# Kernel tuning notes

Hardware: AMD Instinct MI355X
Metric: run time of the kernel (lower is better)

Reference implementation:

```python
import jax, jax.numpy as jnp
import numpy as np

B, N, M = 4, 1024, 3072          # batch, latent (query) len, prefix context len
D, H, DH, L, F = 512, 8, 64, 6, 2048  # dim, heads, dim_head, depth, ff hidden
SCALE = DH ** -0.5


def _ln(x, g, b):
    m = jnp.mean(x, axis=-1, keepdims=True)
    v = jnp.mean(jnp.square(x - m), axis=-1, keepdims=True)
    return (x - m) * jax.lax.rsqrt(v + 1e-5) * g + b


def _heads(t):  # [b, n, h*d] -> [b, h, n, d]
    b, n, _ = t.shape
    return t.reshape(b, n, H, DH).transpose(0, 2, 1, 3)


def _attend(q, k, v):
    # q:[b,h,i,d], k/v:[b,h,j,d]; causal mask triu(j-i+1) as in source
    i, j = q.shape[2], k.shape[2]
    sim = jnp.einsum('bhid,bhjd->bhij', q * SCALE, k)
    mask = jnp.triu(jnp.ones((i, j), dtype=bool), j - i + 1)
    sim = jnp.where(mask, -jnp.finfo(sim.dtype).max, sim)
    attn = jax.nn.softmax(sim, axis=-1)
    out = jnp.einsum('bhij,bhjd->bhid', attn, v)
    return out.transpose(0, 2, 1, 3).reshape(q.shape[0], i, H * DH)


def _ff(x, g, b, w1, w2):
    return jax.nn.gelu(_ln(x, g, b) @ w1, approximate=False) @ w2


def setup_inputs() -> dict:
    key = jax.random.key(0)
    ks = jax.random.split(key, 12)
    rn = lambda k, shape: jax.random.normal(k, shape, dtype=jnp.float32) * 0.02
    return {
        'x': jax.random.normal(ks[0], (B, N, D), jnp.float32),
        'context': jax.random.normal(ks[1], (B, M, D), jnp.float32),
        'pa_norm_g': jnp.ones((D,), jnp.float32), 'pa_norm_b': jnp.zeros((D,), jnp.float32),
        'pa_cnorm_g': jnp.ones((D,), jnp.float32), 'pa_cnorm_b': jnp.zeros((D,), jnp.float32),
        'pa_wq': rn(ks[2], (D, H * DH)), 'pa_wkv': rn(ks[3], (D, 2 * H * DH)),
        'pa_wo': rn(ks[4], (H * DH, D)), 'pa_wo_b': jnp.zeros((D,), jnp.float32),
        'pf_ln_g': jnp.ones((D,), jnp.float32), 'pf_ln_b': jnp.zeros((D,), jnp.float32),
        'pf_w1': rn(ks[5], (D, F)), 'pf_w2': rn(ks[6], (F, D)),
        'sa_ln_g': jnp.ones((L, D), jnp.float32), 'sa_ln_b': jnp.zeros((L, D), jnp.float32),
        'sa_wqkv': rn(ks[7], (L, D, 3 * H * DH)), 'sa_wo': rn(ks[8], (L, H * DH, D)),
        'sf_ln_g': jnp.ones((L, D), jnp.float32), 'sf_ln_b': jnp.zeros((L, D), jnp.float32),
        'sf_w1': rn(ks[9], (L, D, F)), 'sf_w2': rn(ks[10], (L, F, D)),
    }


def reference(x, context, pa_norm_g, pa_norm_b, pa_cnorm_g, pa_cnorm_b,
              pa_wq, pa_wkv, pa_wo, pa_wo_b, pf_ln_g, pf_ln_b, pf_w1, pf_w2,
              sa_ln_g, sa_ln_b, sa_wqkv, sa_wo, sf_ln_g, sf_ln_b, sf_w1, sf_w2):
    # --- CausalPrefixAttention (eval mode: no dropout, context_mask=None) ---
    xn = _ln(x, pa_norm_g, pa_norm_b)
    cn = _ln(context, pa_cnorm_g, pa_cnorm_b)
    q = _heads(xn @ pa_wq)
    k_in, v_in = jnp.split(xn @ pa_wkv, 2, axis=-1)
    k_c, v_c = jnp.split(cn @ pa_wkv, 2, axis=-1)
    k = _heads(jnp.concatenate([k_c, k_in], axis=1))  # [b,h,M+N,d]
    v = _heads(jnp.concatenate([v_c, v_in], axis=1))
    x = _attend(q, k, v) @ pa_wo + pa_wo_b + x
    x = _ff(x, pf_ln_g, pf_ln_b, pf_w1, pf_w2) + x
    # --- depth x (CausalAttention + FeedForward) ---
    for l in range(L):
        xn = _ln(x, sa_ln_g[l], sa_ln_b[l])
        qq, kk, vv = jnp.split(xn @ sa_wqkv[l], 3, axis=-1)
        x = _attend(_heads(qq), _heads(kk), _heads(vv)) @ sa_wo[l] + x
        x = _ff(x, sf_ln_g[l], sf_ln_b[l], sf_w1[l], sf_w2[l]) + x
    return x
```

## Files before the change

kernel.cpp:

```cpp
#include <hip/hip_runtime.h>
#include <hip/hip_bf16.h>
#include <cstdint>
#include <cstddef>

typedef __bf16 bf16;
typedef __attribute__((ext_vector_type(8))) __bf16 bf16x8;
typedef __attribute__((ext_vector_type(4))) __bf16 bf16x4;
typedef __attribute__((ext_vector_type(4))) float f32x4;

constexpr int B_ = 4, QN = 1024, MCTX = 3072, D_ = 512, H_ = 8, DHE = 64, L_ = 6, FF_ = 2048;
constexpr float SCL2_ = 0.18033688011f;

__device__ __forceinline__ f32x4 mfma16(bf16x8 a, bf16x8 b, f32x4 c) {
  return __builtin_amdgcn_mfma_f32_16x16x32_bf16(a, b, c, 0, 0, 0);
}

__device__ __forceinline__ void gl_lds16(const bf16* g, bf16* l) {
  __builtin_amdgcn_global_load_lds((const __attribute__((address_space(1))) void*)g,
                                   (__attribute__((address_space(3))) void*)l, 16, 0, 0);
}

__device__ __forceinline__ float fexp2(float x) {
  float r;
  asm("v_exp_f32 %0, %1" : "=v"(r) : "v"(x));
  return r;
}

__global__ __launch_bounds__(256) void ln_kernel(const float* __restrict__ x,
                                                 const float* __restrict__ g,
                                                 const float* __restrict__ b,
                                                 bf16* __restrict__ out, int rows) {
  int wid = threadIdx.x >> 6, lane = threadIdx.x & 63;
  int row = blockIdx.x * 4 + wid;
  if (row >= rows) return;
  const float* xr = x + (size_t)row * D_;
  f32x4 a0 = *(const f32x4*)(xr + lane * 8);
  f32x4 a1 = *(const f32x4*)(xr + lane * 8 + 4);
  float s = 0.f;
#pragma unroll
  for (int i = 0; i < 4; i++) { s += a0[i]; s += a1[i]; }
#pragma unroll
  for (int d = 1; d < 64; d <<= 1) s += __shfl_xor(s, d);
  float mean = s * (1.0f / 512.0f);
  float q = 0.f;
#pragma unroll
  for (int i = 0; i < 4; i++) {
    float t0 = a0[i] - mean, t1 = a1[i] - mean;
    q += t0 * t0 + t1 * t1;
  }
#pragma unroll
  for (int d = 1; d < 64; d <<= 1) q += __shfl_xor(q, d);
  float rstd = rsqrtf(q * (1.0f / 512.0f) + 1e-5f);
  f32x4 g0 = *(const f32x4*)(g + lane * 8);
  f32x4 g1 = *(const f32x4*)(g + lane * 8 + 4);
  f32x4 b0 = *(const f32x4*)(b + lane * 8);
  f32x4 b1 = *(const f32x4*)(b + lane * 8 + 4);
  bf16x8 o;
#pragma unroll
  for (int i = 0; i < 4; i++) {
    o[i] = (bf16)((a0[i] - mean) * rstd * g0[i] + b0[i]);
    o[i + 4] = (bf16)((a1[i] - mean) * rstd * g1[i] + b1[i]);
  }
  *(bf16x8*)(out + (size_t)row * D_ + lane * 8) = o;
}

struct WDesc { const float* src; bf16* dst; int K; int N; int tstart; };
struct WPack { WDesc d[30]; int n; };

__global__ __launch_bounds__(256) void wtrans_all(WPack p) {
  __shared__ float tile[64][65];
  const int bid = blockIdx.x;
  int mi = 0;
  for (int i = 1; i < p.n; i++)
    if (p.d[i].tstart <= bid) mi = i;
  const float* src = p.d[mi].src;
  bf16* dst = p.d[mi].dst;
  const int K = p.d[mi].K, N = p.d[mi].N;
  const int lt = bid - p.d[mi].tstart;
  const int ntx = N >> 6;
  const int n0 = (lt % ntx) * 64, k0 = (lt / ntx) * 64;
  const int tx = threadIdx.x, ty = threadIdx.y;
#pragma unroll
  for (int pp = 0; pp < 16; pp++)
    tile[pp * 4 + ty][tx] = src[(size_t)(k0 + pp * 4 + ty) * N + n0 + tx];
  __syncthreads();
#pragma unroll
  for (int pp = 0; pp < 16; pp++)
    dst[(size_t)(n0 + pp * 4 + ty) * K + k0 + tx] = (bf16)tile[tx][pp * 4 + ty];
}

template <int EPI>
__global__ __launch_bounds__(256) void gemm128(const bf16* __restrict__ A,
                                               const bf16* __restrict__ BT,
                                               void* __restrict__ C0,
                                               void* __restrict__ C1,
                                               void* __restrict__ C2,
                                               const float* __restrict__ resid,
                                               const float* __restrict__ bias,
                                               int M, int N, int K, int vstr) {
  __shared__ bf16 sm[6 * 4096];
  bf16* sA = sm;
  bf16* sB = sm + 3 * 4096;
  const int tid = threadIdx.x, wid = tid >> 6, lane = tid & 63;
  const int lr = lane & 15, lg = lane >> 4;
  const int tm = blockIdx.y * 128, tn = blockIdx.x * 128;
  const int wr = (wid >> 1) * 64, wc = (wid & 1) * 64;

  const int r0 = tid >> 2, ls0 = tid & 3;
  const int gs0 = ls0 ^ (r0 & 3);
  const bf16* gA0 = A + (size_t)(tm + r0) * K + gs0 * 8;
  const bf16* gB0 = BT + (size_t)(tn + r0) * K + gs0 * 8;
  const bf16* gA1 = gA0 + (size_t)64 * K;
  const bf16* gB1 = gB0 + (size_t)64 * K;

  f32x4 acc[4][4] = {};
  const int nt = K >> 5;

  auto stage = [&](int bi, int kt) {
    gl_lds16(gA0 + kt, sA + bi * 4096 + tid * 8);
    gl_lds16(gA1 + kt, sA + bi * 4096 + (tid + 256) * 8);
    gl_lds16(gB0 + kt, sB + bi * 4096 + tid * 8);
    gl_lds16(gB1 + kt, sB + bi * 4096 + (tid + 256) * 8);
  };

  stage(0, 0);
  stage(1, 32);

  for (int t = 0; t < nt; ++t) {
    const int bi = t % 3;
    if (t + 1 < nt) {
      asm volatile("s_waitcnt vmcnt(4)" ::: "memory");
    } else {
      asm volatile("s_waitcnt vmcnt(0)" ::: "memory");
    }
    __builtin_amdgcn_s_barrier();
    __builtin_amdgcn_sched_barrier(0);
    if (t + 2 < nt) stage((t + 2) % 3, (t + 2) * 32);

    bf16x8 af[4], bfr[4];
#pragma unroll
    for (int i = 0; i < 4; i++) {
      const int row = wr + i * 16 + lr;
      af[i] = *(const bf16x8*)&sA[bi * 4096 + row * 32 + ((lg ^ (row & 3)) * 8)];
    }
#pragma unroll
    for (int j = 0; j < 4; j++) {
      const int row = wc + j * 16 + lr;
      bfr[j] = *(const bf16x8*)&sB[bi * 4096 + row * 32 + ((lg ^ (row & 3)) * 8)];
    }
#pragma unroll
    for (int i = 0; i < 4; i++)
#pragma unroll
      for (int j = 0; j < 4; j++)
        acc[i][j] = mfma16(af[i], bfr[j], acc[i][j]);
  }

  const bool row_major_dst =
      (EPI == 1) || (EPI == 3 && tn < 1024) || (EPI == 4 && tn < 1024) || (EPI == 5 && tn < 512);
  if (row_major_dst) {
    bf16* dst;
    int dstr, rbase, coff;
    if (EPI == 1) { dst = (bf16*)C0; dstr = N; rbase = tm; coff = tn; }
    else if (EPI == 3) {
      if (tn < 512) { dst = (bf16*)C0; dstr = 512; rbase = tm; coff = tn; }
      else { dst = (bf16*)C1; dstr = 1024; rbase = (tm >> 10) * 4096 + (tm & 1023) + 3072; coff = tn - 512; }
    } else if (EPI == 4) { dst = (bf16*)C0; dstr = 1536; rbase = tm; coff = tn; }
    else { dst = (bf16*)C1; dstr = 1024; rbase = (tm / 3072) * 4096 + (tm % 3072); coff = tn; }

    __syncthreads();
    bf16* lb = sm;
#pragma unroll
    for (int i = 0; i < 4; i++) {
#pragma unroll
      for (int r = 0; r < 4; r++) {
        const int row = wr + i * 16 + lg * 4 + r;
#pragma unroll
        for (int j = 0; j < 4; j++) {
          const int col = wc + j * 16 + lr;
          float v = acc[i][j][r];
          if (EPI == 1) {
            float u = v * (0.7978845608f + 0.0356774081f * v * v);
            float e = fexp2(fminf(2.885390082f * u, 80.0f));
            v = v * e / (1.0f + e);
          }
          lb[row * 128 + (col ^ ((row & 7) << 3))] = (bf16)v;
        }
      }
    }
    __syncthreads();
#pragma unroll
    for (int p = 0; p < 8; p++) {
      const int row = p * 16 + (tid >> 4);
      const int cb = (tid & 15) * 8;
      bf16x8 v = *(const bf16x8*)&lb[row * 128 + (cb ^ ((row & 7) << 3))];
      *(bf16x8*)&dst[(size_t)(rbase + row) * dstr + coff + cb] = v;
    }
  } else {
#pragma unroll
    for (int i = 0; i < 4; i++) {
      const int row = tm + wr + i * 16 + lg * 4;
#pragma unroll
      for (int j = 0; j < 4; j++) {
        const int col = tn + wc + j * 16 + lr;
        bf16x4 pk = {(bf16)acc[i][j][0], (bf16)acc[i][j][1],
                     (bf16)acc[i][j][2], (bf16)acc[i][j][3]};
        if (EPI == 3) {
          const int cc = col - 1024, hh = cc >> 6, dh = cc & 63;
          const int bb = row >> 10, s = (row & 1023) + 3072;
          *(bf16x4*)&((bf16*)C2)[((size_t)(bb * 8 + hh) * 64 + dh) * vstr + s] = pk;
        } else if (EPI == 4) {
          const int cc = col - 1024, hh = cc >> 6, dh = cc & 63;
          const int bb = row >> 10, s = row & 1023;
          *(bf16x4*)&((bf16*)C2)[((size_t)(bb * 8 + hh) * 64 + dh) * vstr + s] = pk;
        } else {
          const int bq = row / 3072, s = row - bq * 3072;
          const int cc = col - 512, hh = cc >> 6, dh = cc & 63;
          *(bf16x4*)&((bf16*)C2)[((size_t)(bq * 8 + hh) * 64 + dh) * vstr + s] = pk;
        }
      }
    }
  }
}

__global__ __launch_bounds__(512) void gemm64k2(const bf16* __restrict__ A,
                                                const bf16* __restrict__ BT,
                                                float* __restrict__ Cout,
                                                const float* __restrict__ resid,
                                                const float* __restrict__ bias,
                                                int M, int N, int K) {
  __shared__ bf16 sm[2][2][64 * 128];
  const int tid = threadIdx.x, wid = tid >> 6, lane = tid & 63;
  const int lr = lane & 15, lg = lane >> 4;
  const int tm = blockIdx.y * 64, tn = blockIdx.x * 64;
  const int ws = wid >> 2;
  const int wq = wid & 3;
  const int wr = (wq >> 1) * 32, wc = (wq & 1) * 32;

  const int r0 = tid >> 4, u0 = tid & 7, h0 = (tid >> 3) & 1;
  const int g0 = h0 * 8 + (u0 ^ (r0 & 7));
  const bf16* gA0 = A + (size_t)(tm + r0) * K + g0 * 8;
  const bf16* gB0 = BT + (size_t)(tn + r0) * K + g0 * 8;
  const bf16* gA1 = gA0 + (size_t)32 * K;
  const bf16* gB1 = gB0 + (size_t)32 * K;

  auto stage = [&](int bi, int kt) {
    gl_lds16(gA0 + kt, &sm[bi][0][tid * 8]);
    gl_lds16(gA1 + kt, &sm[bi][0][(tid + 512) * 8]);
    gl_lds16(gB0 + kt, &sm[bi][1][tid * 8]);
    gl_lds16(gB1 + kt, &sm[bi][1][(tid + 512) * 8]);
  };

  f32x4 acc[2][2] = {};
  const int nt = K >> 7;
  stage(0, 0);
  int buf = 0;
  for (int t = 0; t < nt; ++t) {
    asm volatile("s_waitcnt vmcnt(0)" ::: "memory");
    __builtin_amdgcn_s_barrier();
    __builtin_amdgcn_sched_barrier(0);
    if (t + 1 < nt) stage(buf ^ 1, (t + 1) * 128);

    bf16x8 af[2][2], bfr[2][2];
#pragma unroll
    for (int i = 0; i < 2; i++) {
      const int row = wr + i * 16 + lr;
#pragma unroll
      for (int kk = 0; kk < 2; kk++) {
        const int slot = ws * 8 + ((kk * 4 + lg) ^ (row & 7));
        af[i][kk] = *(const bf16x8*)&sm[buf][0][row * 128 + slot * 8];
      }
    }
#pragma unroll
    for (int j = 0; j < 2; j++) {
      const int row = wc + j * 16 + lr;
#pragma unroll
      for (int kk = 0; kk < 2; kk++) {
        const int slot = ws * 8 + ((kk * 4 + lg) ^ (row & 7));
        bfr[j][kk] = *(const bf16x8*)&sm[buf][1][row * 128 + slot * 8];
      }
    }
#pragma unroll
    for (int kk = 0; kk < 2; kk++)
#pragma unroll
      for (int i = 0; i < 2; i++)
#pragma unroll
        for (int j = 0; j < 2; j++)
          acc[i][j] = mfma16(af[i][kk], bfr[j][kk], acc[i][j]);
    buf ^= 1;
  }

  __syncthreads();
  float* lbuf = (float*)&sm[0][0][0];
  if (ws == 0) {
#pragma unroll
    for (int i = 0; i < 2; i++)
#pragma unroll
      for (int r = 0; r < 4; r++) {
        const int row = wr + i * 16 + lg * 4 + r;
#pragma unroll
        for (int j = 0; j < 2; j++)
          lbuf[row * 68 + wc + j * 16 + lr] = acc[i][j][r];
      }
  }
  __syncthreads();
  if (ws == 1) {
#pragma unroll
    for (int i = 0; i < 2; i++)
#pragma unroll
      for (int r = 0; r < 4; r++) {
        const int row = wr + i * 16 + lg * 4 + r;
#pragma unroll
        for (int j = 0; j < 2; j++)
          lbuf[row * 68 + wc + j * 16 + lr] += acc[i][j][r];
      }
  }
  __syncthreads();
#pragma unroll
  for (int p = 0; p < 2; p++) {
    const int row = p * 32 + (tid >> 4);
    const int col = (tid & 15) * 4;
    f32x4 v = *(const f32x4*)&lbuf[row * 68 + col];
    const size_t gidx = (size_t)(tm + row) * N + tn + col;
    f32x4 rs = *(const f32x4*)&resid[gidx];
    if (bias) {
      f32x4 bs = *(const f32x4*)&bias[tn + col];
#pragma unroll
      for (int e = 0; e < 4; e++) v[e] += bs[e];
    }
#pragma unroll
    for (int e = 0; e < 4; e++) v[e] += rs[e];
    *(f32x4*)&Cout[gidx] = v;
  }
}

template <int NSPLIT>
__global__ __launch_bounds__(512) void attn_kernel(const bf16* __restrict__ q, int qstride,
                                                   const bf16* __restrict__ k, int kstride,
                                                   const bf16* __restrict__ vt,
                                                   bf16* __restrict__ out,
                                                   bf16* __restrict__ po,
                                                   float* __restrict__ pm,
                                                   float* __restrict__ pl,
                                                   int Skv, int Moff, int spllen) {
  __shared__ bf16 kls[2][4096];
  __shared__ bf16 vls[2][4096];
  __shared__ bf16 pls[8][1024];

  const int tid = threadIdx.x, wid = tid >> 6, lane = tid & 63;
  const int lr = lane & 15, lg = lane >> 4, lg4 = lg * 4;
  const int b = blockIdx.z, h = blockIdx.y;
  const int qblk = blockIdx.x / NSPLIT;
  const int split = blockIdx.x % NSPLIT;
  const int q0b = qblk * 128;
  const int q0w = q0b + wid * 16;
  const int kv_lo = split * spllen;

  int jhi_blk = Moff + q0b + 127;
  if (jhi_blk > Skv - 1) jhi_blk = Skv - 1;
  int hi = kv_lo + spllen;
  if (hi > jhi_blk + 1) hi = jhi_blk + 1;
  const int ntl = (hi > kv_lo) ? ((hi - kv_lo + 63) >> 6) : 0;

  if (NSPLIT > 1 && ntl == 0) {
    size_t rb = ((size_t)split * B_ * H_ + (size_t)b * H_ + h) * QN + q0w;
    const int row = lane >> 2;
    bf16x8 z = {};
#pragma unroll
    for (int half = 0; half < 2; half++)
      *(bf16x8*)&po[(rb + row) * 64 + (lane & 3) * 16 + half * 8] = z;
    if (lg == 0) { pm[rb + lr] = -3e38f; pl[rb + lr] = 0.f; }
    return;
  }

  const int sel = ((tid >> 6) & 1) * 32 + ((tid >> 4) & 3) * 8;
  const int srow0 = (tid >> 7) * 16 + (tid & 15);
  const bf16* kbase = k + (size_t)b * Skv * kstride + h * DHE + sel;
  const bf16* vbase = vt + (size_t)((b * H_ + h) * DHE) * Skv + sel;

  const bf16* qp = q + (size_t)(b * QN + q0w + lr) * qstride + h * DHE;
  bf16x8 qa0 = *(const bf16x8*)(qp + lg * 8);
  bf16x8 qa1 = *(const bf16x8*)(qp + 32 + lg * 8);
#pragma unroll
  for (int i = 0; i < 8; i++) {
    qa0[i] = (bf16)((float)qa0[i] * SCL2_);
    qa1[i] = (bf16)((float)qa1[i] * SCL2_);
  }
  bf16x8 vones;
#pragma unroll
  for (int i = 0; i < 8; i++) vones[i] = (bf16)1.0f;

  f32x4 o[4] = {};
  f32x4 o4 = {};

  auto stage = [&](int bi, int j0) {
    gl_lds16(kbase + (size_t)(j0 + srow0) * kstride, &kls[bi][tid * 8]);
    gl_lds16(vbase + (size_t)srow0 * Skv + j0, &vls[bi][tid * 8]);
  };

  stage(0, kv_lo);
  __syncthreads();
  int buf = 0;
  bf16* pw = &pls[wid][0];

  for (int t = 0; t < ntl; ++t) {
    const int j0 = kv_lo + t * 64;
    if (t + 1 < ntl) stage(buf ^ 1, j0 + 64);
    const bf16* kbp = &kls[buf][0];
    const bf16* vbp = &vls[buf][0];

    f32x4 sv[4];
    __builtin_amdgcn_s_setprio(1);
#pragma unroll
    for (int kg = 0; kg < 4; kg++) {
      bf16x8 k0 = *(const bf16x8*)(kbp + (kg * 128 + lane) * 8);
      bf16x8 k1 = *(const bf16x8*)(kbp + (kg * 128 + 64 + lane) * 8);
      f32x4 z = {0.f, 0.f, 0.f, 0.f};
      z = mfma16(k0, qa0, z);
      z = mfma16(k1, qa1, z);
      sv[kg] = z;
    }
    __builtin_amdgcn_s_setprio(0);
    const bool full = (j0 + 63 <= Moff + q0w);
    if (!full) {
      const int limq = Moff + q0w + lr;
#pragma unroll
      for (int kg = 0; kg < 4; kg++)
#pragma unroll
        for (int r = 0; r < 4; r++)
          if (j0 + kg * 16 + lg4 + r > limq) sv[kg][r] = -3e38f;
    }
#pragma unroll
    for (int kg = 0; kg < 4; kg++) {
      float p0 = fexp2(sv[kg][0]);
      float p1 = fexp2(sv[kg][1]);
      float p2 = fexp2(sv[kg][2]);
      float p3 = fexp2(sv[kg][3]);
      bf16x4 pk = {(bf16)p0, (bf16)p1, (bf16)p2, (bf16)p3};
      const int k8 = kg * 2 + (lg >> 1);
      *(bf16x4*)(pw + ((k8 >> 2) * 64 + (k8 & 3) * 16 + lr) * 8 + (lg & 1) * 4) = pk;
    }
    bf16x8 pa0 = *(const bf16x8*)(pw + lane * 8);
    bf16x8 pa1 = *(const bf16x8*)(pw + (64 + lane) * 8);
    __builtin_amdgcn_s_setprio(1);
#pragma unroll
    for (int f = 0; f < 4; f++) {
      bf16x8 v0 = *(const bf16x8*)(vbp + (f * 128 + lane) * 8);
      bf16x8 v1 = *(const bf16x8*)(vbp + (f * 128 + 64 + lane) * 8);
      o[f] = mfma16(pa0, v0, o[f]);
      o[f] = mfma16(pa1, v1, o[f]);
    }
    o4 = mfma16(pa0, vones, o4);
    o4 = mfma16(pa1, vones, o4);
    __builtin_amdgcn_s_setprio(0);
    __syncthreads();
    buf ^= 1;
  }

  if (NSPLIT == 1) {
    float li[4];
#pragma unroll
    for (int r = 0; r < 4; r++) li[r] = 1.0f / o4[r];
#pragma unroll
    for (int f = 0; f < 4; f++)
#pragma unroll
      for (int r = 0; r < 4; r++) {
        const int row = lg4 + r, col = f * 16 + lr;
        pw[row * 64 + (col ^ ((row & 7) << 3))] = (bf16)(o[f][r] * li[r]);
      }
    const int row = lane >> 2;
#pragma unroll
    for (int half = 0; half < 2; half++) {
      const int cb = (lane & 3) * 16 + half * 8;
      bf16x8 v = *(const bf16x8*)&pw[row * 64 + (cb ^ ((row & 7) << 3))];
      *(bf16x8*)&out[(size_t)(b * QN + q0w + row) * D_ + h * DHE + cb] = v;
    }
  } else {
    size_t rb = ((size_t)split * B_ * H_ + (size_t)b * H_ + h) * QN + q0w;
#pragma unroll
    for (int f = 0; f < 4; f++)
#pragma unroll
      for (int r = 0; r < 4; r++) {
        const int row = lg4 + r, col = f * 16 + lr;
        pw[row * 64 + (col ^ ((row & 7) << 3))] = (bf16)o[f][r];
      }
    const int row = lane >> 2;
#pragma unroll
    for (int half = 0; half < 2; half++) {
      const int cb = (lane & 3) * 16 + half * 8;
      bf16x8 v = *(const bf16x8*)&pw[row * 64 + (cb ^ ((row & 7) << 3))];
      *(bf16x8*)&po[(rb + row) * 64 + cb] = v;
    }
    if (lr == 0) {
#pragma unroll
      for (int r = 0; r < 4; r++) {
        pm[rb + lg4 + r] = 0.f;
        pl[rb + lg4 + r] = o4[r];
      }
    }
  }
}

template <int NSPLIT>
__global__ __launch_bounds__(256) void attn_combine(const bf16* __restrict__ po,
                                                    const float* __restrict__ pm,
                                                    const float* __restrict__ pl,
                                                    bf16* __restrict__ out) {
  constexpr int TOT = B_ * H_ * QN;
  const int wid = threadIdx.x >> 6, lane = threadIdx.x & 63;
  const int row = blockIdx.x * 4 + wid;
  float mv[NSPLIT], lv[NSPLIT];
  float mstar = -3e38f;
#pragma unroll
  for (int s = 0; s < NSPLIT; s++) {
    mv[s] = pm[s * TOT + row];
    lv[s] = pl[s * TOT + row];
    mstar = fmaxf(mstar, mv[s]);
  }
  float lstar = 0.f, acc = 0.f;
#pragma unroll
  for (int s = 0; s < NSPLIT; s++) {
    float w = fexp2(mv[s] - mstar);
    lstar += lv[s] * w;
    acc += (float)po[((size_t)s * TOT + row) * 64 + lane] * w;
  }
  const int b = row >> 13, hq = row & 8191, h = hq >> 10, qq = hq & 1023;
  out[((size_t)b * QN + qq) * D_ + h * DHE + lane] = (bf16)(acc / lstar);
}

extern "C" void kernel_launch(void* const* d_in, const int* in_sizes, int n_in,
                              void* d_out, int out_size, void* d_ws, size_t ws_size,
                              hipStream_t stream) {
  const float* x       = (const float*)d_in[0];
  const float* ctx     = (const float*)d_in[1];
  const float* pa_ng   = (const float*)d_in[2];
  const float* pa_nb   = (const float*)d_in[3];
  const float* pa_cg   = (const float*)d_in[4];
  const float* pa_cb   = (const float*)d_in[5];
  const float* pa_wq   = (const float*)d_in[6];
  const float* pa_wkv  = (const float*)d_in[7];
  const float* pa_wo   = (const float*)d_in[8];
  const float* pa_wob  = (const float*)d_in[9];
  const float* pf_g    = (const float*)d_in[10];
  const float* pf_b    = (const float*)d_in[11];
  const float* pf_w1   = (const float*)d_in[12];
  const float* pf_w2   = (const float*)d_in[13];
  const float* sa_g    = (const float*)d_in[14];
  const float* sa_b    = (const float*)d_in[15];
  const float* sa_wqkv = (const float*)d_in[16];
  const float* sa_wo   = (const float*)d_in[17];
  const float* sf_g    = (const float*)d_in[18];
  const float* sf_b    = (const float*)d_in[19];
  const float* sf_w1   = (const float*)d_in[20];
  const float* sf_w2   = (const float*)d_in[21];
  float* xo = (float*)d_out;

  char* ws = (char*)d_ws;
  size_t off = 0;
  auto alloc = [&](size_t bytes) -> char* {
    char* p = ws + off;
    off += (bytes + 255) & ~(size_t)255;
    return p;
  };

  bf16* wqT    = (bf16*)alloc((size_t)512 * 512 * 2);
  bf16* wkvT   = (bf16*)alloc((size_t)1024 * 512 * 2);
  bf16* woT    = (bf16*)alloc((size_t)512 * 512 * 2);
  bf16* w1T    = (bf16*)alloc((size_t)2048 * 512 * 2);
  bf16* w2T    = (bf16*)alloc((size_t)512 * 2048 * 2);
  bf16* saqkvT = (bf16*)alloc((size_t)L_ * 1536 * 512 * 2);
  bf16* sawoT  = (bf16*)alloc((size_t)L_ * 512 * 512 * 2);
  bf16* sfw1T  = (bf16*)alloc((size_t)L_ * 2048 * 512 * 2);
  bf16* sfw2T  = (bf16*)alloc((size_t)L_ * 512 * 2048 * 2);
  bf16* xn    = (bf16*)alloc((size_t)4096 * 512 * 2);
  bf16* reg1  = (bf16*)alloc((size_t)12288 * 512 * 2);
  bf16* qb    = (bf16*)alloc((size_t)4096 * 512 * 2);
  bf16* reg2  = (bf16*)alloc((size_t)B_ * 4096 * 1024 * 2);
  bf16* vtb   = (bf16*)alloc((size_t)B_ * H_ * 64 * 4096 * 2);
  bf16* attnb = (bf16*)alloc((size_t)4096 * 512 * 2);
  constexpr int NSPL = 4;
  constexpr int TOTR = B_ * H_ * QN;
  bf16* po = (bf16*)alloc((size_t)NSPL * TOTR * 64 * 2);
  float* pmb = (float*)alloc((size_t)NSPL * TOTR * 4);
  float* plb = (float*)alloc((size_t)NSPL * TOTR * 4);
  const bool use_split = (off <= ws_size);
  bf16* cn = reg1;
  bf16* qkvb = reg1;
  bf16* kvb = reg2;
  bf16* ffh = reg2;
  (void)in_sizes; (void)n_in; (void)out_size;

  WPack wp;
  int nt_acc = 0, wi = 0;
  auto addw = [&](const float* s, bf16* d, int K, int N) {
    wp.d[wi].src = s; wp.d[wi].dst = d; wp.d[wi].K = K; wp.d[wi].N = N;
    wp.d[wi].tstart = nt_acc;
    nt_acc += (N / 64) * (K / 64);
    wi++;
  };
  addw(pa_wq, wqT, 512, 512);
  addw(pa_wkv, wkvT, 512, 1024);
  addw(pa_wo, woT, 512, 512);
  addw(pf_w1, w1T, 512, 2048);
  addw(pf_w2, w2T, 2048, 512);
  for (int l = 0; l < L_; l++) {
    addw(sa_wqkv + (size_t)l * 512 * 1536, saqkvT + (size_t)l * 1536 * 512, 512, 1536);
    addw(sa_wo + (size_t)l * 512 * 512, sawoT + (size_t)l * 512 * 512, 512, 512);
    addw(sf_w1 + (size_t)l * 512 * 2048, sfw1T + (size_t)l * 2048 * 512, 512, 2048);
    addw(sf_w2 + (size_t)l * 2048 * 512, sfw2T + (size_t)l * 512 * 2048, 2048, 512);
  }
  wp.n = wi;
  wtrans_all<<<nt_acc, dim3(64, 4, 1), 0, stream>>>(wp);

  ln_kernel<<<1024, 256, 0, stream>>>(x, pa_ng, pa_nb, xn, 4096);
  ln_kernel<<<3072, 256, 0, stream>>>(ctx, pa_cg, pa_cb, cn, 12288);
  hipLaunchKernelGGL(HIP_KERNEL_NAME(gemm128<5>), dim3(1024 / 128, 12288 / 128), dim3(256), 0,
                     stream, cn, wkvT, nullptr, kvb, vtb, nullptr, nullptr, 12288, 1024, 512, 4096);
  hipLaunchKernelGGL(HIP_KERNEL_NAME(gemm128<3>), dim3(1536 / 128, 4096 / 128), dim3(256), 0,
                     stream, xn, wqT, qb, kvb, vtb, nullptr, nullptr, 4096, 1536, 512, 4096);
  if (use_split) {
    hipLaunchKernelGGL(HIP_KERNEL_NAME(attn_kernel<NSPL>), dim3((QN / 128) * NSPL, H_, B_), dim3(512), 0,
                       stream, qb, 512, kvb, 1024, vtb, attnb, po, pmb, plb, 4096, MCTX, 1024);
    hipLaunchKernelGGL(HIP_KERNEL_NAME(attn_combine<NSPL>), dim3(TOTR / 4), dim3(256), 0,
                       stream, po, pmb, plb, attnb);
  } else {
    hipLaunchKernelGGL(HIP_KERNEL_NAME(attn_kernel<1>), dim3(QN / 128, H_, B_), dim3(512), 0,
                       stream, qb, 512, kvb, 1024, vtb, attnb, po, pmb, plb, 4096, MCTX, 4096);
  }
  gemm64k2<<<dim3(512 / 64, 4096 / 64), 512, 0, stream>>>(attnb, woT, xo, x, pa_wob, 4096, 512, 512);
  ln_kernel<<<1024, 256, 0, stream>>>(xo, pf_g, pf_b, xn, 4096);
  hipLaunchKernelGGL(HIP_KERNEL_NAME(gemm128<1>), dim3(2048 / 128, 4096 / 128), dim3(256), 0,
                     stream, xn, w1T, ffh, nullptr, nullptr, nullptr, nullptr, 4096, 2048, 512, 0);
  gemm64k2<<<dim3(512 / 64, 4096 / 64), 512, 0, stream>>>(ffh, w2T, xo, xo, nullptr, 4096, 512, 2048);

  for (int l = 0; l < L_; l++) {
    ln_kernel<<<1024, 256, 0, stream>>>(xo, sa_g + l * 512, sa_b + l * 512, xn, 4096);
    hipLaunchKernelGGL(HIP_KERNEL_NAME(gemm128<4>), dim3(1536 / 128, 4096 / 128), dim3(256), 0,
                       stream, xn, saqkvT + (size_t)l * 1536 * 512, qkvb, nullptr, vtb,
                       nullptr, nullptr, 4096, 1536, 512, 1024);
    if (use_split) {
      hipLaunchKernelGGL(HIP_KERNEL_NAME(attn_kernel<2>), dim3((QN / 128) * 2, H_, B_), dim3(512), 0,
                         stream, qkvb, 1536, qkvb + 512, 1536, vtb, attnb, po, pmb, plb, 1024, 0, 512);
      hipLaunchKernelGGL(HIP_KERNEL_NAME(attn_combine<2>), dim3(TOTR / 4), dim3(256), 0,
                         stream, po, pmb, plb, attnb);
    } else {
      hipLaunchKernelGGL(HIP_KERNEL_NAME(attn_kernel<1>), dim3(QN / 128, H_, B_), dim3(512), 0,
                         stream, qkvb, 1536, qkvb + 512, 1536, vtb, attnb, po, pmb, plb, 1024, 0, 1024);
    }
    gemm64k2<<<dim3(512 / 64, 4096 / 64), 512, 0, stream>>>(attnb, sawoT + (size_t)l * 512 * 512,
                                                            xo, xo, nullptr, 4096, 512, 512);
    ln_kernel<<<1024, 256, 0, stream>>>(xo, sf_g + l * 512, sf_b + l * 512, xn, 4096);
    hipLaunchKernelGGL(HIP_KERNEL_NAME(gemm128<1>), dim3(2048 / 128, 4096 / 128), dim3(256), 0,
                       stream, xn, sfw1T + (size_t)l * 2048 * 512, ffh, nullptr, nullptr,
                       nullptr, nullptr, 4096, 2048, 512, 0);
    gemm64k2<<<dim3(512 / 64, 4096 / 64), 512, 0, stream>>>(ffh, sfw2T + (size_t)l * 512 * 2048,
                                                            xo, xo, nullptr, 4096, 512, 2048);
  }
}
```

Measured before the change: 752.7 us.

## Fuse split-KV attention combine into attention kernel; triple-buffer gemm64k2 K loop

The separate attn_combine launch is removed. Each split block now publishes its partial output and row sum, then bumps a per-group atomic counter, and the last block to arrive reduces the splits and writes the final output. The unused running-max buffer is dropped and counters are zeroed once with a memset. Separately, gemm64k2 moves from a double-buffered 128-wide K tile to a triple-buffered 64-wide K tile with vmcnt(2) waits, so loads stay in flight across iterations. This trades the extra kernel launches and combine passes for atomics and threadfences, and adds more barrier iterations in the GEMM.

```diff
diff --git a/kernel.cpp b/kernel.cpp
--- a/kernel.cpp
+++ b/kernel.cpp
@@ -228,7 +228,7 @@
                                                 const float* __restrict__ resid,
                                                 const float* __restrict__ bias,
                                                 int M, int N, int K) {
-  __shared__ bf16 sm[2][2][64 * 128];
+  __shared__ bf16 sm[3][2][64 * 64];
   const int tid = threadIdx.x, wid = tid >> 6, lane = tid & 63;
   const int lr = lane & 15, lg = lane >> 4;
   const int tm = blockIdx.y * 64, tn = blockIdx.x * 64;
@@ -236,57 +236,48 @@
   const int wq = wid & 3;
   const int wr = (wq >> 1) * 32, wc = (wq & 1) * 32;
 
-  const int r0 = tid >> 4, u0 = tid & 7, h0 = (tid >> 3) & 1;
-  const int g0 = h0 * 8 + (u0 ^ (r0 & 7));
+  const int r0 = tid >> 3, u0 = tid & 7;
+  const int g0 = u0 ^ (r0 & 7);
   const bf16* gA0 = A + (size_t)(tm + r0) * K + g0 * 8;
   const bf16* gB0 = BT + (size_t)(tn + r0) * K + g0 * 8;
-  const bf16* gA1 = gA0 + (size_t)32 * K;
-  const bf16* gB1 = gB0 + (size_t)32 * K;
 
   auto stage = [&](int bi, int kt) {
     gl_lds16(gA0 + kt, &sm[bi][0][tid * 8]);
-    gl_lds16(gA1 + kt, &sm[bi][0][(tid + 512) * 8]);
     gl_lds16(gB0 + kt, &sm[bi][1][tid * 8]);
-    gl_lds16(gB1 + kt, &sm[bi][1][(tid + 512) * 8]);
   };
 
   f32x4 acc[2][2] = {};
-  const int nt = K >> 7;
+  const int nt = K >> 6;
   stage(0, 0);
-  int buf = 0;
+  if (nt > 1) stage(1, 64);
+
   for (int t = 0; t < nt; ++t) {
-    asm volatile("s_waitcnt vmcnt(0)" ::: "memory");
+    const int bi = t % 3;
+    if (t + 1 < nt) {
+      asm volatile("s_waitcnt vmcnt(2)" ::: "memory");
+    } else {
+      asm volatile("s_waitcnt vmcnt(0)" ::: "memory");
+    }
     __builtin_amdgcn_s_barrier();
     __builtin_amdgcn_sched_barrier(0);
-    if (t + 1 < nt) stage(buf ^ 1, (t + 1) * 128);
-
-    bf16x8 af[2][2], bfr[2][2];
+    if (t + 2 < nt) stage((t + 2) % 3, (t + 2) * 64);
+
+    bf16x8 af[2], bfr[2];
 #pragma unroll
     for (int i = 0; i < 2; i++) {
       const int row = wr + i * 16 + lr;
-#pragma unroll
-      for (int kk = 0; kk < 2; kk++) {
-        const int slot = ws * 8 + ((kk * 4 + lg) ^ (row & 7));
-        af[i][kk] = *(const bf16x8*)&sm[buf][0][row * 128 + slot * 8];
-      }
+      af[i] = *(const bf16x8*)&sm[bi][0][row * 64 + (((ws * 4 + lg) ^ (row & 7)) * 8)];
     }
 #pragma unroll
     for (int j = 0; j < 2; j++) {
       const int row = wc + j * 16 + lr;
-#pragma unroll
-      for (int kk = 0; kk < 2; kk++) {
-        const int slot = ws * 8 + ((kk * 4 + lg) ^ (row & 7));
-        bfr[j][kk] = *(const bf16x8*)&sm[buf][1][row * 128 + slot * 8];
-      }
-    }
-#pragma unroll
-    for (int kk = 0; kk < 2; kk++)
-#pragma unroll
-      for (int i = 0; i < 2; i++)
-#pragma unroll
-        for (int j = 0; j < 2; j++)
-          acc[i][j] = mfma16(af[i][kk], bfr[j][kk], acc[i][j]);
-    buf ^= 1;
+      bfr[j] = *(const bf16x8*)&sm[bi][1][row * 64 + (((ws * 4 + lg) ^ (row & 7)) * 8)];
+    }
+#pragma unroll
+    for (int i = 0; i < 2; i++)
+#pragma unroll
+      for (int j = 0; j < 2; j++)
+        acc[i][j] = mfma16(af[i], bfr[j], acc[i][j]);
   }
 
   __syncthreads();
@@ -339,12 +330,13 @@
                                                    const bf16* __restrict__ vt,
                                                    bf16* __restrict__ out,
                                                    bf16* __restrict__ po,
-                                                   float* __restrict__ pm,
                                                    float* __restrict__ pl,
+                                                   unsigned* __restrict__ cnt,
                                                    int Skv, int Moff, int spllen) {
   __shared__ bf16 kls[2][4096];
   __shared__ bf16 vls[2][4096];
   __shared__ bf16 pls[8][1024];
+  __shared__ unsigned scnt_sh;
 
   const int tid = threadIdx.x, wid = tid >> 6, lane = tid & 63;
   const int lr = lane & 15, lg = lane >> 4, lg4 = lg * 4;
@@ -354,6 +346,7 @@
   const int q0b = qblk * 128;
   const int q0w = q0b + wid * 16;
   const int kv_lo = split * spllen;
+  constexpr int TOT = B_ * H_ * QN;
 
   int jhi_blk = Moff + q0b + 127;
   if (jhi_blk > Skv - 1) jhi_blk = Skv - 1;
@@ -362,169 +355,176 @@
   const int ntl = (hi > kv_lo) ? ((hi - kv_lo + 63) >> 6) : 0;
 
   if (NSPLIT > 1 && ntl == 0) {
-    size_t rb = ((size_t)split * B_ * H_ + (size_t)b * H_ + h) * QN + q0w;
+    size_t rb = ((size_t)split * TOT + (size_t)(b * H_ + h) * QN + q0w);
     const int row = lane >> 2;
     bf16x8 z = {};
 #pragma unroll
     for (int half = 0; half < 2; half++)
       *(bf16x8*)&po[(rb + row) * 64 + (lane & 3) * 16 + half * 8] = z;
-    if (lg == 0) { pm[rb + lr] = -3e38f; pl[rb + lr] = 0.f; }
-    return;
-  }
-
-  const int sel = ((tid >> 6) & 1) * 32 + ((tid >> 4) & 3) * 8;
-  const int srow0 = (tid >> 7) * 16 + (tid & 15);
-  const bf16* kbase = k + (size_t)b * Skv * kstride + h * DHE + sel;
-  const bf16* vbase = vt + (size_t)((b * H_ + h) * DHE) * Skv + sel;
-
-  const bf16* qp = q + (size_t)(b * QN + q0w + lr) * qstride + h * DHE;
-  bf16x8 qa0 = *(const bf16x8*)(qp + lg * 8);
-  bf16x8 qa1 = *(const bf16x8*)(qp + 32 + lg * 8);
-#pragma unroll
-  for (int i = 0; i < 8; i++) {
-    qa0[i] = (bf16)((float)qa0[i] * SCL2_);
-    qa1[i] = (bf16)((float)qa1[i] * SCL2_);
-  }
-  bf16x8 vones;
-#pragma unroll
-  for (int i = 0; i < 8; i++) vones[i] = (bf16)1.0f;
-
-  f32x4 o[4] = {};
-  f32x4 o4 = {};
-
-  auto stage = [&](int bi, int j0) {
-    gl_lds16(kbase + (size_t)(j0 + srow0) * kstride, &kls[bi][tid * 8]);
-    gl_lds16(vbase + (size_t)srow0 * Skv + j0, &vls[bi][tid * 8]);
-  };
-
-  stage(0, kv_lo);
-  __syncthreads();
-  int buf = 0;
-  bf16* pw = &pls[wid][0];
-
-  for (int t = 0; t < ntl; ++t) {
-    const int j0 = kv_lo + t * 64;
-    if (t + 1 < ntl) stage(buf ^ 1, j0 + 64);
-    const bf16* kbp = &kls[buf][0];
-    const bf16* vbp = &vls[buf][0];
-
-    f32x4 sv[4];
-    __builtin_amdgcn_s_setprio(1);
-#pragma unroll
-    for (int kg = 0; kg < 4; kg++) {
-      bf16x8 k0 = *(const bf16x8*)(kbp + (kg * 128 + lane) * 8);
-      bf16x8 k1 = *(const bf16x8*)(kbp + (kg * 128 + 64 + lane) * 8);
-      f32x4 z = {0.f, 0.f, 0.f, 0.f};
-      z = mfma16(k0, qa0, z);
-      z = mfma16(k1, qa1, z);
-      sv[kg] = z;
-    }
-    __builtin_amdgcn_s_setprio(0);
-    const bool full = (j0 + 63 <= Moff + q0w);
-    if (!full) {
-      const int limq = Moff + q0w + lr;
-#pragma unroll
-      for (int kg = 0; kg < 4; kg++)
-#pragma unroll
-        for (int r = 0; r < 4; r++)
-          if (j0 + kg * 16 + lg4 + r > limq) sv[kg][r] = -3e38f;
-    }
-#pragma unroll
-    for (int kg = 0; kg < 4; kg++) {
-      float p0 = fexp2(sv[kg][0]);
-      float p1 = fexp2(sv[kg][1]);
-      float p2 = fexp2(sv[kg][2]);
-      float p3 = fexp2(sv[kg][3]);
-      bf16x4 pk = {(bf16)p0, (bf16)p1, (bf16)p2, (bf16)p3};
-      const int k8 = kg * 2 + (lg >> 1);
-      *(bf16x4*)(pw + ((k8 >> 2) * 64 + (k8 & 3) * 16 + lr) * 8 + (lg & 1) * 4) = pk;
-    }
-    bf16x8 pa0 = *(const bf16x8*)(pw + lane * 8);
-    bf16x8 pa1 = *(const bf16x8*)(pw + (64 + lane) * 8);
-    __builtin_amdgcn_s_setprio(1);
-#pragma unroll
-    for (int f = 0; f < 4; f++) {
-      bf16x8 v0 = *(const bf16x8*)(vbp + (f * 128 + lane) * 8);
-      bf16x8 v1 = *(const bf16x8*)(vbp + (f * 128 + 64 + lane) * 8);
-      o[f] = mfma16(pa0, v0, o[f]);
-      o[f] = mfma16(pa1, v1, o[f]);
-    }
-    o4 = mfma16(pa0, vones, o4);
-    o4 = mfma16(pa1, vones, o4);
-    __builtin_amdgcn_s_setprio(0);
+    if (lr == 0) {
+#pragma unroll
+      for (int r = 0; r < 4; r++) pl[rb + lg4 + r] = 0.f;
+    }
+  } else {
+    const int sel = ((tid >> 6) & 1) * 32 + ((tid >> 4) & 3) * 8;
+    const int srow0 = (tid >> 7) * 16 + (tid & 15);
+    const bf16* kbase = k + (size_t)b * Skv * kstride + h * DHE + sel;
+    const bf16* vbase = vt + (size_t)((b * H_ + h) * DHE) * Skv + sel;
+
+    const bf16* qp = q + (size_t)(b * QN + q0w + lr) * qstride + h * DHE;
+    bf16x8 qa0 = *(const bf16x8*)(qp + lg * 8);
+    bf16x8 qa1 = *(const bf16x8*)(qp + 32 + lg * 8);
+#pragma unroll
+    for (int i = 0; i < 8; i++) {
+      qa0[i] = (bf16)((float)qa0[i] * SCL2_);
+      qa1[i] = (bf16)((float)qa1[i] * SCL2_);
+    }
+    bf16x8 vones;
+#pragma unroll
+    for (int i = 0; i < 8; i++) vones[i] = (bf16)1.0f;
+
+    f32x4 o[4] = {};
+    f32x4 o4 = {};
+
+    auto stage = [&](int bi, int j0) {
+      gl_lds16(kbase + (size_t)(j0 + srow0) * kstride, &kls[bi][tid * 8]);
+      gl_lds16(vbase + (size_t)srow0 * Skv + j0, &vls[bi][tid * 8]);
+    };
+
+    stage(0, kv_lo);
     __syncthreads();
-    buf ^= 1;
-  }
-
-  if (NSPLIT == 1) {
-    float li[4];
-#pragma unroll
-    for (int r = 0; r < 4; r++) li[r] = 1.0f / o4[r];
-#pragma unroll
-    for (int f = 0; f < 4; f++)
-#pragma unroll
-      for (int r = 0; r < 4; r++) {
-        const int row = lg4 + r, col = f * 16 + lr;
-        pw[row * 64 + (col ^ ((row & 7) << 3))] = (bf16)(o[f][r] * li[r]);
-      }
-    const int row = lane >> 2;
-#pragma unroll
-    for (int half = 0; half < 2; half++) {
-      const int cb = (lane & 3) * 16 + half * 8;
-      bf16x8 v = *(const bf16x8*)&pw[row * 64 + (cb ^ ((row & 7) << 3))];
-      *(bf16x8*)&out[(size_t)(b * QN + q0w + row) * D_ + h * DHE + cb] = v;
-    }
-  } else {
-    size_t rb = ((size_t)split * B_ * H_ + (size_t)b * H_ + h) * QN + q0w;
-#pragma unroll
-    for (int f = 0; f < 4; f++)
-#pragma unroll
-      for (int r = 0; r < 4; r++) {
-        const int row = lg4 + r, col = f * 16 + lr;
-        pw[row * 64 + (col ^ ((row & 7) << 3))] = (bf16)o[f][r];
-      }
-    const int row = lane >> 2;
-#pragma unroll
-    for (int half = 0; half < 2; half++) {
-      const int cb = (lane & 3) * 16 + half * 8;
-      bf16x8 v = *(const bf16x8*)&pw[row * 64 + (cb ^ ((row & 7) << 3))];
-      *(bf16x8*)&po[(rb + row) * 64 + cb] = v;
-    }
-    if (lr == 0) {
-#pragma unroll
-      for (int r = 0; r < 4; r++) {
-        pm[rb + lg4 + r] = 0.f;
-        pl[rb + lg4 + r] = o4[r];
-      }
-    }
-  }
-}
-
-template <int NSPLIT>
-__global__ __launch_bounds__(256) void attn_combine(const bf16* __restrict__ po,
-                                                    const float* __restrict__ pm,
-                                                    const float* __restrict__ pl,
-                                                    bf16* __restrict__ out) {
-  constexpr int TOT = B_ * H_ * QN;
-  const int wid = threadIdx.x >> 6, lane = threadIdx.x & 63;
-  const int row = blockIdx.x * 4 + wid;
-  float mv[NSPLIT], lv[NSPLIT];
-  float mstar = -3e38f;
-#pragma unroll
-  for (int s = 0; s < NSPLIT; s++) {
-    mv[s] = pm[s * TOT + row];
-    lv[s] = pl[s * TOT + row];
-    mstar = fmaxf(mstar, mv[s]);
-  }
-  float lstar = 0.f, acc = 0.f;
-#pragma unroll
-  for (int s = 0; s < NSPLIT; s++) {
-    float w = fexp2(mv[s] - mstar);
-    lstar += lv[s] * w;
-    acc += (float)po[((size_t)s * TOT + row) * 64 + lane] * w;
-  }
-  const int b = row >> 13, hq = row & 8191, h = hq >> 10, qq = hq & 1023;
-  out[((size_t)b * QN + qq) * D_ + h * DHE + lane] = (bf16)(acc / lstar);
+    int buf = 0;
+    bf16* pw = &pls[wid][0];
+
+    for (int t = 0; t < ntl; ++t) {
+      const int j0 = kv_lo + t * 64;
+      if (t + 1 < ntl) stage(buf ^ 1, j0 + 64);
+      const bf16* kbp = &kls[buf][0];
+      const bf16* vbp = &vls[buf][0];
+
+      f32x4 sv[4];
+      __builtin_amdgcn_s_setprio(1);
+#pragma unroll
+      for (int kg = 0; kg < 4; kg++) {
+        bf16x8 k0 = *(const bf16x8*)(kbp + (kg * 128 + lane) * 8);
+        bf16x8 k1 = *(const bf16x8*)(kbp + (kg * 128 + 64 + lane) * 8);
+        f32x4 z = {0.f, 0.f, 0.f, 0.f};
+        z = mfma16(k0, qa0, z);
+        z = mfma16(k1, qa1, z);
+        sv[kg] = z;
+      }
+      __builtin_amdgcn_s_setprio(0);
+      const bool full = (j0 + 63 <= Moff + q0w);
+      if (!full) {
+        const int limq = Moff + q0w + lr;
+#pragma unroll
+        for (int kg = 0; kg < 4; kg++)
+#pragma unroll
+          for (int r = 0; r < 4; r++)
+            if (j0 + kg * 16 + lg4 + r > limq) sv[kg][r] = -3e38f;
+      }
+#pragma unroll
+      for (int kg = 0; kg < 4; kg++) {
+        float p0 = fexp2(sv[kg][0]);
+        float p1 = fexp2(sv[kg][1]);
+        float p2 = fexp2(sv[kg][2]);
+        float p3 = fexp2(sv[kg][3]);
+        bf16x4 pk = {(bf16)p0, (bf16)p1, (bf16)p2, (bf16)p3};
+        const int k8 = kg * 2 + (lg >> 1);
+        *(bf16x4*)(pw + ((k8 >> 2) * 64 + (k8 & 3) * 16 + lr) * 8 + (lg & 1) * 4) = pk;
+      }
+      bf16x8 pa0 = *(const bf16x8*)(pw + lane * 8);
+      bf16x8 pa1 = *(const bf16x8*)(pw + (64 + lane) * 8);
+      __builtin_amdgcn_s_setprio(1);
+#pragma unroll
+      for (int f = 0; f < 4; f++) {
+        bf16x8 v0 = *(const bf16x8*)(vbp + (f * 128 + lane) * 8);
+        bf16x8 v1 = *(const bf16x8*)(vbp + (f * 128 + 64 + lane) * 8);
+        o[f] = mfma16(pa0, v0, o[f]);
+        o[f] = mfma16(pa1, v1, o[f]);
+      }
+      o4 = mfma16(pa0, vones, o4);
+      o4 = mfma16(pa1, vones, o4);
+      __builtin_amdgcn_s_setprio(0);
+      __syncthreads();
+      buf ^= 1;
+    }
+
+    if (NSPLIT == 1) {
+      float li[4];
+#pragma unroll
+      for (int r = 0; r < 4; r++) li[r] = 1.0f / o4[r];
+#pragma unroll
+      for (int f = 0; f < 4; f++)
+#pragma unroll
+        for (int r = 0; r < 4; r++) {
+          const int row = lg4 + r, col = f * 16 + lr;
+          pw[row * 64 + (col ^ ((row & 7) << 3))] = (bf16)(o[f][r] * li[r]);
+        }
+      const int row = lane >> 2;
+#pragma unroll
+      for (int half = 0; half < 2; half++) {
+        const int cb = (lane & 3) * 16 + half * 8;
+        bf16x8 v = *(const bf16x8*)&pw[row * 64 + (cb ^ ((row & 7) << 3))];
+        *(bf16x8*)&out[(size_t)(b * QN + q0w + row) * D_ + h * DHE + cb] = v;
+      }
+    } else {
+      size_t rb = ((size_t)split * TOT + (size_t)(b * H_ + h) * QN + q0w);
+#pragma unroll
+      for (int f = 0; f < 4; f++)
+#pragma unroll
+        for (int r = 0; r < 4; r++) {
+          const int row = lg4 + r, col = f * 16 + lr;
+          pw[row * 64 + (col ^ ((row & 7) << 3))] = (bf16)o[f][r];
+        }
+      const int row = lane >> 2;
+#pragma unroll
+      for (int half = 0; half < 2; half++) {
+        const int cb = (lane & 3) * 16 + half * 8;
+        bf16x8 v = *(const bf16x8*)&pw[row * 64 + (cb ^ ((row & 7) << 3))];
+        *(bf16x8*)&po[(rb + row) * 64 + cb] = v;
+      }
+      if (lr == 0) {
+#pragma unroll
+        for (int r = 0; r < 4; r++) pl[rb + lg4 + r] = o4[r];
+      }
+    }
+  }
+
+  if (NSPLIT > 1) {
+    __threadfence();
+    __syncthreads();
+    if (tid == 0)
+      scnt_sh = atomicAdd(&cnt[(unsigned)((b * H_ + h) * (QN / 128) + qblk)], 1u);
+    __syncthreads();
+    if (scnt_sh == NSPLIT - 1) {
+      __threadfence();
+      const int row = tid >> 2;
+      const int cb = (tid & 3) * 16;
+      const size_t base = (size_t)(b * H_ + h) * QN + q0b + row;
+      float l = 0.f;
+      float a0[8] = {}, a1[8] = {};
+#pragma unroll
+      for (int s = 0; s < NSPLIT; s++) {
+        const size_t pr = (size_t)s * TOT + base;
+        l += pl[pr];
+        bf16x8 v0 = *(const bf16x8*)&po[pr * 64 + cb];
+        bf16x8 v1 = *(const bf16x8*)&po[pr * 64 + cb + 8];
+#pragma unroll
+        for (int j = 0; j < 8; j++) { a0[j] += (float)v0[j]; a1[j] += (float)v1[j]; }
+      }
+      const float inv = 1.0f / l;
+      bf16x8 w0, w1;
+#pragma unroll
+      for (int j = 0; j < 8; j++) {
+        w0[j] = (bf16)(a0[j] * inv);
+        w1[j] = (bf16)(a1[j] * inv);
+      }
+      bf16* op = &out[((size_t)b * QN + q0b + row) * D_ + h * DHE + cb];
+      *(bf16x8*)op = w0;
+      *(bf16x8*)(op + 8) = w1;
+    }
+  }
 }
 
 extern "C" void kernel_launch(void* const* d_in, const int* in_sizes, int n_in,
@@ -579,15 +579,18 @@
   bf16* attnb = (bf16*)alloc((size_t)4096 * 512 * 2);
   constexpr int NSPL = 4;
   constexpr int TOTR = B_ * H_ * QN;
+  constexpr int NGRP = B_ * H_ * (QN / 128);
   bf16* po = (bf16*)alloc((size_t)NSPL * TOTR * 64 * 2);
-  float* pmb = (float*)alloc((size_t)NSPL * TOTR * 4);
   float* plb = (float*)alloc((size_t)NSPL * TOTR * 4);
+  unsigned* cntb = (unsigned*)alloc((size_t)7 * NGRP * 4);
   const bool use_split = (off <= ws_size);
   bf16* cn = reg1;
   bf16* qkvb = reg1;
   bf16* kvb = reg2;
   bf16* ffh = reg2;
   (void)in_sizes; (void)n_in; (void)out_size;
+
+  if (use_split) hipMemsetAsync(cntb, 0, (size_t)7 * NGRP * 4, stream);
 
   WPack wp;
   int nt_acc = 0, wi = 0;
@@ -619,12 +622,10 @@
                      stream, xn, wqT, qb, kvb, vtb, nullptr, nullptr, 4096, 1536, 512, 4096);
   if (use_split) {
     hipLaunchKernelGGL(HIP_KERNEL_NAME(attn_kernel<NSPL>), dim3((QN / 128) * NSPL, H_, B_), dim3(512), 0,
-                       stream, qb, 512, kvb, 1024, vtb, attnb, po, pmb, plb, 4096, MCTX, 1024);
-    hipLaunchKernelGGL(HIP_KERNEL_NAME(attn_combine<NSPL>), dim3(TOTR / 4), dim3(256), 0,
-                       stream, po, pmb, plb, attnb);
+                       stream, qb, 512, kvb, 1024, vtb, attnb, po, plb, cntb, 4096, MCTX, 1024);
   } else {
     hipLaunchKernelGGL(HIP_KERNEL_NAME(attn_kernel<1>), dim3(QN / 128, H_, B_), dim3(512), 0,
-                       stream, qb, 512, kvb, 1024, vtb, attnb, po, pmb, plb, 4096, MCTX, 4096);
+                       stream, qb, 512, kvb, 1024, vtb, attnb, po, plb, (unsigned*)nullptr, 4096, MCTX, 4096);
   }
   gemm64k2<<<dim3(512 / 64, 4096 / 64), 512, 0, stream>>>(attnb, woT, xo, x, pa_wob, 4096, 512, 512);
   ln_kernel<<<1024, 256, 0, stream>>>(xo, pf_g, pf_b, xn, 4096);
@@ -639,12 +640,12 @@
                        nullptr, nullptr, 4096, 1536, 512, 1024);
     if (use_split) {
       hipLaunchKernelGGL(HIP_KERNEL_NAME(attn_kernel<2>), dim3((QN / 128) * 2, H_, B_), dim3(512), 0,
-                         stream, qkvb, 1536, qkvb + 512, 1536, vtb, attnb, po, pmb, plb, 1024, 0, 512);
-      hipLaunchKernelGGL(HIP_KERNEL_NAME(attn_combine<2>), dim3(TOTR / 4), dim3(256), 0,
-                         stream, po, pmb, plb, attnb);
+                         stream, qkvb, 1536, qkvb + 512, 1536, vtb, attnb, po, plb,
+                         cntb + (size_t)(1 + l) * NGRP, 1024, 0, 512);
     } else {
       hipLaunchKernelGGL(HIP_KERNEL_NAME(attn_kernel<1>), dim3(QN / 128, H_, B_), dim3(512), 0,
-                         stream, qkvb, 1536, qkvb + 512, 1536, vtb, attnb, po, pmb, plb, 1024, 0, 1024);
+                         stream, qkvb, 1536, qkvb + 512, 1536, vtb, attnb, po, plb,
+                         (unsigned*)nullptr, 1024, 0, 1024);
     }
     gemm64k2<<<dim3(512 / 64, 4096 / 64), 512, 0, stream>>>(attnb, sawoT + (size_t)l * 512 * 512,
                                                             xo, xo, nullptr, 4096, 512, 512);
```

Measured after the change: 2.373 ms. +215.2%, slower.

## Switch gemm64k2 to triple-buffered 64-wide K tiles with deeper prefetch

Applied to the files above, without the earlier changes.

Changes the split-K GEMM from a double buffer of 128-wide K tiles to a triple buffer of 64-wide K tiles. Loads are issued two stages ahead, and the wait drops from vmcnt(0) to vmcnt(2), so global-to-LDS loads overlap more of the MFMA work. The trade-off is twice as many loop iterations and barriers, with fewer MFMAs per barrier. LDS use falls from 64KB to 48KB, which may allow more blocks per CU.

```diff
diff --git a/kernel.cpp b/kernel.cpp
--- a/kernel.cpp
+++ b/kernel.cpp
@@ -228,7 +228,7 @@
                                                 const float* __restrict__ resid,
                                                 const float* __restrict__ bias,
                                                 int M, int N, int K) {
-  __shared__ bf16 sm[2][2][64 * 128];
+  __shared__ bf16 sm[3][2][64 * 64];
   const int tid = threadIdx.x, wid = tid >> 6, lane = tid & 63;
   const int lr = lane & 15, lg = lane >> 4;
   const int tm = blockIdx.y * 64, tn = blockIdx.x * 64;
@@ -236,57 +236,48 @@
   const int wq = wid & 3;
   const int wr = (wq >> 1) * 32, wc = (wq & 1) * 32;
 
-  const int r0 = tid >> 4, u0 = tid & 7, h0 = (tid >> 3) & 1;
-  const int g0 = h0 * 8 + (u0 ^ (r0 & 7));
+  const int r0 = tid >> 3, u0 = tid & 7;
+  const int g0 = u0 ^ (r0 & 7);
   const bf16* gA0 = A + (size_t)(tm + r0) * K + g0 * 8;
   const bf16* gB0 = BT + (size_t)(tn + r0) * K + g0 * 8;
-  const bf16* gA1 = gA0 + (size_t)32 * K;
-  const bf16* gB1 = gB0 + (size_t)32 * K;
 
   auto stage = [&](int bi, int kt) {
     gl_lds16(gA0 + kt, &sm[bi][0][tid * 8]);
-    gl_lds16(gA1 + kt, &sm[bi][0][(tid + 512) * 8]);
     gl_lds16(gB0 + kt, &sm[bi][1][tid * 8]);
-    gl_lds16(gB1 + kt, &sm[bi][1][(tid + 512) * 8]);
   };
 
   f32x4 acc[2][2] = {};
-  const int nt = K >> 7;
+  const int nt = K >> 6;
   stage(0, 0);
-  int buf = 0;
+  if (nt > 1) stage(1, 64);
+
   for (int t = 0; t < nt; ++t) {
-    asm volatile("s_waitcnt vmcnt(0)" ::: "memory");
+    const int bi = t % 3;
+    if (t + 1 < nt) {
+      asm volatile("s_waitcnt vmcnt(2)" ::: "memory");
+    } else {
+      asm volatile("s_waitcnt vmcnt(0)" ::: "memory");
+    }
     __builtin_amdgcn_s_barrier();
     __builtin_amdgcn_sched_barrier(0);
-    if (t + 1 < nt) stage(buf ^ 1, (t + 1) * 128);
-
-    bf16x8 af[2][2], bfr[2][2];
+    if (t + 2 < nt) stage((t + 2) % 3, (t + 2) * 64);
+
+    bf16x8 af[2], bfr[2];
 #pragma unroll
     for (int i = 0; i < 2; i++) {
       const int row = wr + i * 16 + lr;
-#pragma unroll
-      for (int kk = 0; kk < 2; kk++) {
-        const int slot = ws * 8 + ((kk * 4 + lg) ^ (row & 7));
-        af[i][kk] = *(const bf16x8*)&sm[buf][0][row * 128 + slot * 8];
-      }
+      af[i] = *(const bf16x8*)&sm[bi][0][row * 64 + (((ws * 4 + lg) ^ (row & 7)) * 8)];
     }
 #pragma unroll
     for (int j = 0; j < 2; j++) {
       const int row = wc + j * 16 + lr;
-#pragma unroll
-      for (int kk = 0; kk < 2; kk++) {
-        const int slot = ws * 8 + ((kk * 4 + lg) ^ (row & 7));
-        bfr[j][kk] = *(const bf16x8*)&sm[buf][1][row * 128 + slot * 8];
-      }
-    }
-#pragma unroll
-    for (int kk = 0; kk < 2; kk++)
-#pragma unroll
-      for (int i = 0; i < 2; i++)
-#pragma unroll
-        for (int j = 0; j < 2; j++)
-          acc[i][j] = mfma16(af[i][kk], bfr[j][kk], acc[i][j]);
-    buf ^= 1;
+      bfr[j] = *(const bf16x8*)&sm[bi][1][row * 64 + (((ws * 4 + lg) ^ (row & 7)) * 8)];
+    }
+#pragma unroll
+    for (int i = 0; i < 2; i++)
+#pragma unroll
+      for (int j = 0; j < 2; j++)
+        acc[i][j] = mfma16(af[i], bfr[j], acc[i][j]);
   }
 
   __syncthreads();
```

After: 754.5 us. Within noise of the previous version (+0.2%).
